# Optimization experiments

Measured on AMD Instinct MI355X. Metric: run time of the kernel, lower is better.

Reference implementation:

```python
import jax, jax.numpy as jnp
import numpy as np

B, L, C, D = 4, 2048, 64, 4


def setup_inputs() -> dict:
    key = jax.random.key(0)
    k1, k2, k3, k4 = jax.random.split(key, 4)
    # |A| kept < ~0.92 so the length-2048 recurrence stays bounded
    A_re = jax.random.uniform(k1, (B, L, C, D), jnp.float32, -0.65, 0.65)
    A_im = jax.random.uniform(k2, (B, L, C, D), jnp.float32, -0.65, 0.65)
    X_re = jax.random.normal(k3, (B, L, C, D, D), jnp.float32)
    X_im = jax.random.normal(k4, (B, L, C, D, D), jnp.float32)
    return {"A_re": A_re, "A_im": A_im, "X_re": X_re, "X_im": X_im}


def _combine(c1, c2):
    # first-order linear recurrence combine: (a, x) o (b, y) = (b*a, b*x + y)
    a1, x1 = c1
    a2, x2 = c2
    return a2 * a1, a2 * x1 + x2


def reference(A_re, A_im, X_re, X_im):
    # Diagonal complex pscan: Y[t] = A[t] * Y[t-1] + X[t], elementwise,
    # with diagonal A [B,L,C,D] broadcast over the trailing D dim of X [B,L,C,D,D]
    A = (A_re + 1j * A_im).astype(jnp.complex64)[..., None]  # [B,L,C,D,1]
    X = (X_re + 1j * X_im).astype(jnp.complex64)             # [B,L,C,D,D]
    _, Y = jax.lax.associative_scan(_combine, (A, X), axis=1)
    # return real view [B,L,C,D,D,2] (real, imag) like torch.view_as_real
    return jnp.stack([Y.real, Y.imag], axis=-1)
```

## Files before the change

### kernel.cpp

```cpp
#include <hip/hip_runtime.h>

#define BB 4
#define LL 2048
#define CC 64
#define DD 4
#define NN (CC * DD * DD)
#define GG 32
#define TT (LL / GG)


__global__ __launch_bounds__(256) void pscan_phase1(
    const float* __restrict__ A_re, const float* __restrict__ A_im,
    const float* __restrict__ X_re, const float* __restrict__ X_im,
    float4* __restrict__ agg) {
  int u = blockIdx.x * 256 + threadIdx.x;
  int n  = u & (NN - 1);
  int bg = u >> 10;
  int g  = bg & (GG - 1);
  int b  = bg >> 5;
  int t0 = g * TT;
  long baseA = (long)(b * LL + t0) * (CC * DD) + (n >> 2);
  long baseX = (long)(b * LL + t0) * NN + n;

  float p_re = 1.f, p_im = 0.f, s_re = 0.f, s_im = 0.f;
#pragma unroll 8
  for (int t = 0; t < TT; ++t) {
    float are = A_re[baseA + (long)t * (CC * DD)];
    float aim = A_im[baseA + (long)t * (CC * DD)];
    float xre = X_re[baseX + (long)t * NN];
    float xim = X_im[baseX + (long)t * NN];
    float nsre = are * s_re - aim * s_im + xre;
    float nsim = are * s_im + aim * s_re + xim;
    float npre = are * p_re - aim * p_im;
    float npim = are * p_im + aim * p_re;
    s_re = nsre; s_im = nsim; p_re = npre; p_im = npim;
  }
  agg[u] = make_float4(p_re, p_im, s_re, s_im);
}

__global__ __launch_bounds__(256) void pscan_phase2(float4* __restrict__ agg) {
  int u = blockIdx.x * 256 + threadIdx.x;
  int n = u & (NN - 1);
  int b = u >> 10;
  float rp_re = 1.f, rp_im = 0.f, rs_re = 0.f, rs_im = 0.f;
  for (int g = 0; g < GG; ++g) {
    long idx = (long)(b * GG + g) * NN + n;
    float4 v = agg[idx];
    agg[idx] = make_float4(rp_re, rp_im, rs_re, rs_im);
    float np_re = v.x * rp_re - v.y * rp_im;
    float np_im = v.x * rp_im + v.y * rp_re;
    float ns_re = v.x * rs_re - v.y * rs_im + v.z;
    float ns_im = v.x * rs_im + v.y * rs_re + v.w;
    rp_re = np_re; rp_im = np_im; rs_re = ns_re; rs_im = ns_im;
  }
}

__global__ __launch_bounds__(256) void pscan_phase3(
    const float* __restrict__ A_re, const float* __restrict__ A_im,
    const float* __restrict__ X_re, const float* __restrict__ X_im,
    const float4* __restrict__ carry, float2* __restrict__ out) {
  int u = blockIdx.x * 256 + threadIdx.x;
  int n  = u & (NN - 1);
  int bg = u >> 10;
  int g  = bg & (GG - 1);
  int b  = bg >> 5;
  int t0 = g * TT;
  long baseA = (long)(b * LL + t0) * (CC * DD) + (n >> 2);
  long baseX = (long)(b * LL + t0) * NN + n;

  float4 cv = carry[u];
  float y_re = cv.z, y_im = cv.w;
#pragma unroll 8
  for (int t = 0; t < TT; ++t) {
    float are = A_re[baseA + (long)t * (CC * DD)];
    float aim = A_im[baseA + (long)t * (CC * DD)];
    float xre = X_re[baseX + (long)t * NN];
    float xim = X_im[baseX + (long)t * NN];
    float ny_re = are * y_re - aim * y_im + xre;
    float ny_im = are * y_im + aim * y_re + xim;
    y_re = ny_re; y_im = ny_im;
    out[baseX + (long)t * NN] = make_float2(y_re, y_im);
  }
}

extern "C" void kernel_launch(void* const* d_in, const int* in_sizes, int n_in,
                              void* d_out, int out_size, void* d_ws, size_t ws_size,
                              hipStream_t stream) {
  const float* A_re = (const float*)d_in[0];
  const float* A_im = (const float*)d_in[1];
  const float* X_re = (const float*)d_in[2];
  const float* X_im = (const float*)d_in[3];
  float2* out = (float2*)d_out;
  float4* agg = (float4*)d_ws;

  const int total = BB * GG * NN;
  pscan_phase1<<<total / 256, 256, 0, stream>>>(A_re, A_im, X_re, X_im, agg);
  pscan_phase2<<<(BB * NN) / 256, 256, 0, stream>>>(agg);
  pscan_phase3<<<total / 256, 256, 0, stream>>>(A_re, A_im, X_re, X_im, agg, out);
}
```

Baseline: 153.0 us.

## Vectorize pscan over D lanes, share A loads, use wave-shuffle carry scan

Each thread now owns one (c,d) row and handles all four trailing-D elements with float4 loads and stores, so each A value is loaded once instead of four times and memory accesses are wider. The serial carry propagation in phase 2 is replaced by a Kogge-Stone scan across chunk groups using wavefront shuffles. The chunk count is raised to 64 when the workspace allows, which shortens per-thread sequential chains. The cost is more registers per thread and fewer total threads.

```diff
diff --git a/kernel.cpp b/kernel.cpp
--- a/kernel.cpp
+++ b/kernel.cpp
@@ -2,99 +2,160 @@
 
 #define BB 4
 #define LL 2048
-#define CC 64
-#define DD 4
-#define NN (CC * DD * DD)
-#define GG 32
-#define TT (LL / GG)
+#define KK 256
 
 
+template<int G, int LOGG>
 __global__ __launch_bounds__(256) void pscan_phase1(
     const float* __restrict__ A_re, const float* __restrict__ A_im,
-    const float* __restrict__ X_re, const float* __restrict__ X_im,
-    float4* __restrict__ agg) {
-  int u = blockIdx.x * 256 + threadIdx.x;
-  int n  = u & (NN - 1);
-  int bg = u >> 10;
-  int g  = bg & (GG - 1);
-  int b  = bg >> 5;
-  int t0 = g * TT;
-  long baseA = (long)(b * LL + t0) * (CC * DD) + (n >> 2);
-  long baseX = (long)(b * LL + t0) * NN + n;
+    const float4* __restrict__ X4_re, const float4* __restrict__ X4_im,
+    float2* __restrict__ agg_p, float4* __restrict__ agg_s) {
+  constexpr int T = LL / G;
+  int u  = blockIdx.x * 256 + threadIdx.x;
+  int k  = u & (KK - 1);
+  int bg = u >> 8;
+  int g  = bg & (G - 1);
+  int b  = bg >> LOGG;
+  int t0 = g * T;
+  long base = (long)(b * LL + t0) * KK + k;
 
-  float p_re = 1.f, p_im = 0.f, s_re = 0.f, s_im = 0.f;
+  float p_re = 1.f, p_im = 0.f;
+  float s_re[4] = {0.f, 0.f, 0.f, 0.f};
+  float s_im[4] = {0.f, 0.f, 0.f, 0.f};
 #pragma unroll 8
-  for (int t = 0; t < TT; ++t) {
-    float are = A_re[baseA + (long)t * (CC * DD)];
-    float aim = A_im[baseA + (long)t * (CC * DD)];
-    float xre = X_re[baseX + (long)t * NN];
-    float xim = X_im[baseX + (long)t * NN];
-    float nsre = are * s_re - aim * s_im + xre;
-    float nsim = are * s_im + aim * s_re + xim;
-    float npre = are * p_re - aim * p_im;
-    float npim = are * p_im + aim * p_re;
-    s_re = nsre; s_im = nsim; p_re = npre; p_im = npim;
+  for (int t = 0; t < T; ++t) {
+    long idx = base + (long)t * KK;
+    float are = A_re[idx], aim = A_im[idx];
+    float4 xr = X4_re[idx], xi = X4_im[idx];
+    float xrv[4] = {xr.x, xr.y, xr.z, xr.w};
+    float xiv[4] = {xi.x, xi.y, xi.z, xi.w};
+#pragma unroll
+    for (int j = 0; j < 4; ++j) {
+      float nr = fmaf(are, s_re[j], fmaf(-aim, s_im[j], xrv[j]));
+      float ni = fmaf(are, s_im[j], fmaf( aim, s_re[j], xiv[j]));
+      s_re[j] = nr; s_im[j] = ni;
+    }
+    float npr = are * p_re - aim * p_im;
+    float npi = are * p_im + aim * p_re;
+    p_re = npr; p_im = npi;
   }
-  agg[u] = make_float4(p_re, p_im, s_re, s_im);
+  agg_p[u]       = make_float2(p_re, p_im);
+  agg_s[2*u]     = make_float4(s_re[0], s_im[0], s_re[1], s_im[1]);
+  agg_s[2*u + 1] = make_float4(s_re[2], s_im[2], s_re[3], s_im[3]);
 }
 
-__global__ __launch_bounds__(256) void pscan_phase2(float4* __restrict__ agg) {
+template<int G, int LOGG>
+__global__ __launch_bounds__(256) void pscan_phase2(
+    const float2* __restrict__ agg_p, float4* __restrict__ agg_s) {
   int u = blockIdx.x * 256 + threadIdx.x;
-  int n = u & (NN - 1);
-  int b = u >> 10;
-  float rp_re = 1.f, rp_im = 0.f, rs_re = 0.f, rs_im = 0.f;
-  for (int g = 0; g < GG; ++g) {
-    long idx = (long)(b * GG + g) * NN + n;
-    float4 v = agg[idx];
-    agg[idx] = make_float4(rp_re, rp_im, rs_re, rs_im);
-    float np_re = v.x * rp_re - v.y * rp_im;
-    float np_im = v.x * rp_im + v.y * rp_re;
-    float ns_re = v.x * rs_re - v.y * rs_im + v.z;
-    float ns_im = v.x * rs_im + v.y * rs_re + v.w;
-    rp_re = np_re; rp_im = np_im; rs_re = ns_re; rs_im = ns_im;
+  int g = u & (G - 1);
+  int chain = u >> LOGG;
+  int b = chain >> 8;
+  int k = chain & (KK - 1);
+  long idx = (long)(b * G + g) * KK + k;
+
+  float2 p  = agg_p[idx];
+  float4 s01 = agg_s[2*idx], s23 = agg_s[2*idx + 1];
+  float pr = p.x, pi = p.y;
+  float sr[4] = {s01.x, s01.z, s23.x, s23.z};
+  float si[4] = {s01.y, s01.w, s23.y, s23.w};
+
+#pragma unroll
+  for (int d = 1; d < G; d <<= 1) {
+    float plr = __shfl_up(pr, d, 64);
+    float pli = __shfl_up(pi, d, 64);
+    float slr[4], sli[4];
+#pragma unroll
+    for (int j = 0; j < 4; ++j) {
+      slr[j] = __shfl_up(sr[j], d, 64);
+      sli[j] = __shfl_up(si[j], d, 64);
+    }
+    if (g >= d) {
+#pragma unroll
+      for (int j = 0; j < 4; ++j) {
+        float nr = fmaf(pr, slr[j], fmaf(-pi, sli[j], sr[j]));
+        float ni = fmaf(pr, sli[j], fmaf( pi, slr[j], si[j]));
+        sr[j] = nr; si[j] = ni;
+      }
+      float npr = pr * plr - pi * pli;
+      float npi = pr * pli + pi * plr;
+      pr = npr; pi = npi;
+    }
+  }
+  float er[4], ei[4];
+#pragma unroll
+  for (int j = 0; j < 4; ++j) {
+    er[j] = __shfl_up(sr[j], 1, 64);
+    ei[j] = __shfl_up(si[j], 1, 64);
+  }
+  if (g == 0) {
+#pragma unroll
+    for (int j = 0; j < 4; ++j) { er[j] = 0.f; ei[j] = 0.f; }
+  }
+  agg_s[2*idx]     = make_float4(er[0], ei[0], er[1], ei[1]);
+  agg_s[2*idx + 1] = make_float4(er[2], ei[2], er[3], ei[3]);
+}
+
+template<int G, int LOGG>
+__global__ __launch_bounds__(256) void pscan_phase3(
+    const float* __restrict__ A_re, const float* __restrict__ A_im,
+    const float4* __restrict__ X4_re, const float4* __restrict__ X4_im,
+    const float4* __restrict__ agg_s, float4* __restrict__ out4) {
+  constexpr int T = LL / G;
+  int u  = blockIdx.x * 256 + threadIdx.x;
+  int k  = u & (KK - 1);
+  int bg = u >> 8;
+  int g  = bg & (G - 1);
+  int b  = bg >> LOGG;
+  int t0 = g * T;
+  long base = (long)(b * LL + t0) * KK + k;
+
+  float4 c01 = agg_s[2*u], c23 = agg_s[2*u + 1];
+  float yr[4] = {c01.x, c01.z, c23.x, c23.z};
+  float yi[4] = {c01.y, c01.w, c23.y, c23.w};
+#pragma unroll 8
+  for (int t = 0; t < T; ++t) {
+    long idx = base + (long)t * KK;
+    float are = A_re[idx], aim = A_im[idx];
+    float4 xr = X4_re[idx], xi = X4_im[idx];
+    float xrv[4] = {xr.x, xr.y, xr.z, xr.w};
+    float xiv[4] = {xi.x, xi.y, xi.z, xi.w};
+#pragma unroll
+    for (int j = 0; j < 4; ++j) {
+      float nr = fmaf(are, yr[j], fmaf(-aim, yi[j], xrv[j]));
+      float ni = fmaf(are, yi[j], fmaf( aim, yr[j], xiv[j]));
+      yr[j] = nr; yi[j] = ni;
+    }
+    out4[2*idx]     = make_float4(yr[0], yi[0], yr[1], yi[1]);
+    out4[2*idx + 1] = make_float4(yr[2], yi[2], yr[3], yi[3]);
   }
 }
 
-__global__ __launch_bounds__(256) void pscan_phase3(
-    const float* __restrict__ A_re, const float* __restrict__ A_im,
-    const float* __restrict__ X_re, const float* __restrict__ X_im,
-    const float4* __restrict__ carry, float2* __restrict__ out) {
-  int u = blockIdx.x * 256 + threadIdx.x;
-  int n  = u & (NN - 1);
-  int bg = u >> 10;
-  int g  = bg & (GG - 1);
-  int b  = bg >> 5;
-  int t0 = g * TT;
-  long baseA = (long)(b * LL + t0) * (CC * DD) + (n >> 2);
-  long baseX = (long)(b * LL + t0) * NN + n;
-
-  float4 cv = carry[u];
-  float y_re = cv.z, y_im = cv.w;
-#pragma unroll 8
-  for (int t = 0; t < TT; ++t) {
-    float are = A_re[baseA + (long)t * (CC * DD)];
-    float aim = A_im[baseA + (long)t * (CC * DD)];
-    float xre = X_re[baseX + (long)t * NN];
-    float xim = X_im[baseX + (long)t * NN];
-    float ny_re = are * y_re - aim * y_im + xre;
-    float ny_im = are * y_im + aim * y_re + xim;
-    y_re = ny_re; y_im = ny_im;
-    out[baseX + (long)t * NN] = make_float2(y_re, y_im);
-  }
+template<int G, int LOGG>
+static void launch_all(const float* A_re, const float* A_im,
+                       const float4* X4_re, const float4* X4_im,
+                       void* d_ws, float4* out4, hipStream_t stream) {
+  float2* agg_p = (float2*)d_ws;
+  float4* agg_s = (float4*)((char*)d_ws + (size_t)BB * G * KK * sizeof(float2));
+  int blocks = BB * G;
+  pscan_phase1<G, LOGG><<<blocks, 256, 0, stream>>>(A_re, A_im, X4_re, X4_im, agg_p, agg_s);
+  pscan_phase2<G, LOGG><<<blocks, 256, 0, stream>>>(agg_p, agg_s);
+  pscan_phase3<G, LOGG><<<blocks, 256, 0, stream>>>(A_re, A_im, X4_re, X4_im, agg_s, out4);
 }
 
 extern "C" void kernel_launch(void* const* d_in, const int* in_sizes, int n_in,
                               void* d_out, int out_size, void* d_ws, size_t ws_size,
                               hipStream_t stream) {
-  const float* A_re = (const float*)d_in[0];
-  const float* A_im = (const float*)d_in[1];
-  const float* X_re = (const float*)d_in[2];
-  const float* X_im = (const float*)d_in[3];
-  float2* out = (float2*)d_out;
-  float4* agg = (float4*)d_ws;
+  const float*  A_re  = (const float*)d_in[0];
+  const float*  A_im  = (const float*)d_in[1];
+  const float4* X4_re = (const float4*)d_in[2];
+  const float4* X4_im = (const float4*)d_in[3];
+  float4* out4 = (float4*)d_out;
 
-  const int total = BB * GG * NN;
-  pscan_phase1<<<total / 256, 256, 0, stream>>>(A_re, A_im, X_re, X_im, agg);
-  pscan_phase2<<<(BB * NN) / 256, 256, 0, stream>>>(agg);
-  pscan_phase3<<<total / 256, 256, 0, stream>>>(A_re, A_im, X_re, X_im, agg, out);
+  const size_t need64 = (size_t)BB * 64 * KK * (sizeof(float2) + 2 * sizeof(float4));
+  if (ws_size >= need64) {
+    launch_all<64, 6>(A_re, A_im, X4_re, X4_im, d_ws, out4, stream);
+  } else {
+    launch_all<32, 5>(A_re, A_im, X4_re, X4_im, d_ws, out4, stream);
+  }
 }
```

After: 155.4 us. Within noise of the previous version (+1.5%).
